# Optimization experiments

Hardware: AMD Instinct MI355X
Metric: run time of the kernel (lower is better)

The kernel has to match this reference:

```python
import jax, jax.numpy as jnp
import numpy as np

N = 131072      # H*W*batch = 128*128*8 features
D = 256         # feature_dim
P = 64          # proj_dim
E = 260096      # (2*H*W - H - W)*batch edges of the grid graph
G = 8192        # number of groups
SIM_THRESHOLD = 0.5


def setup_inputs() -> dict:
    key = jax.random.key(0)
    k0, k1, k2, k3 = jax.random.split(key, 4)
    features = jax.random.normal(k0, (N, D), dtype=jnp.float32)
    proj_W = jax.random.normal(k1, (D, P), dtype=jnp.float32) / np.sqrt(D)
    edge_index = jax.random.randint(k2, (2, E), 0, N, dtype=jnp.int64)
    group_ids = jax.random.randint(k3, (N,), 0, G, dtype=jnp.int64)
    return {
        "features": features,
        "proj_W": proj_W,
        "edge_index": edge_index,
        "group_ids": group_ids,
        "num_groups": G,
    }


def reference(features, proj_W, edge_index, group_ids, num_groups):
    # Projection: [N, D] @ [D, P] -> [N, P]
    proj = features @ proj_W
    # Pair comparison: gather both endpoints per edge, dot product per edge
    src, dst = edge_index[0], edge_index[1]
    sims = jnp.sum(proj[src] * proj[dst], axis=-1)            # [E]
    edge_logits = jax.nn.sigmoid(sims - SIM_THRESHOLD)        # [E]
    # Group mean pooling: scatter-add features per group, divide by size
    ones = jnp.ones((features.shape[0],), dtype=features.dtype)
    group_sums = jax.ops.segment_sum(features, group_ids, num_segments=num_groups)  # [G, D]
    group_sizes = jax.ops.segment_sum(ones, group_ids, num_segments=num_groups)     # [G]
    group_sizes = jnp.maximum(group_sizes, 1.0)
    group_means = group_sums / group_sizes[:, None]           # [G, D]
    return group_means, edge_logits
```

## Files before the change

kernel.cpp:

```cpp
#include <hip/hip_runtime.h>
#include <math.h>

constexpr int Nn = 131072;
constexpr int Dd = 256;
constexpr int Pp = 64;
constexpr int Gg = 8192;
constexpr int Ee = 260096;
constexpr float SIM_TH = 0.5f;

typedef _Float16 half8 __attribute__((ext_vector_type(8)));
typedef float floatx4 __attribute__((ext_vector_type(4)));

__global__ __launch_bounds__(256) void k_count_wfrag(
    const int* __restrict__ gid, int* __restrict__ cnt,
    const float* __restrict__ W, _Float16* __restrict__ Wf)
{
    const int i = blockIdx.x * 256 + threadIdx.x;
    atomicAdd(&cnt[gid[i]], 1);
    if (i < 16384) {
        const int j = i & 7;
        const int l = (i >> 3) & 63;
        const int t = (i >> 9) & 3;
        const int c = i >> 11;
        const int k = c * 32 + (l >> 4) * 8 + j;
        const int n = t * 16 + (l & 15);
        Wf[i] = (_Float16)W[k * Pp + n];
    }
}

__global__ __launch_bounds__(256) void k_proj(
    const float* __restrict__ A,
    const _Float16* __restrict__ Wf,
    _Float16* __restrict__ C)
{
    const int l = threadIdx.x & 63;
    const int w = threadIdx.x >> 6;
    const int rowbase = blockIdx.x * 64 + w * 16;
    const int am = l & 15;
    const int q  = l >> 4;

    const float* __restrict__ arow = A + (size_t)(rowbase + am) * Dd + q * 8;
    const half8* __restrict__ bfrag = reinterpret_cast<const half8*>(Wf) + l;

    floatx4 acc[4];
#pragma unroll
    for (int t = 0; t < 4; ++t) acc[t] = (floatx4){0.f, 0.f, 0.f, 0.f};

#pragma unroll
    for (int c = 0; c < 8; ++c) {
        const float4 fa = *reinterpret_cast<const float4*>(arow + c * 32);
        const float4 fb = *reinterpret_cast<const float4*>(arow + c * 32 + 4);
        half8 a;
        a[0] = (_Float16)fa.x; a[1] = (_Float16)fa.y;
        a[2] = (_Float16)fa.z; a[3] = (_Float16)fa.w;
        a[4] = (_Float16)fb.x; a[5] = (_Float16)fb.y;
        a[6] = (_Float16)fb.z; a[7] = (_Float16)fb.w;
        const half8 b0 = bfrag[(c * 4 + 0) * 64];
        const half8 b1 = bfrag[(c * 4 + 1) * 64];
        const half8 b2 = bfrag[(c * 4 + 2) * 64];
        const half8 b3 = bfrag[(c * 4 + 3) * 64];
        acc[0] = __builtin_amdgcn_mfma_f32_16x16x32_f16(a, b0, acc[0], 0, 0, 0);
        acc[1] = __builtin_amdgcn_mfma_f32_16x16x32_f16(a, b1, acc[1], 0, 0, 0);
        acc[2] = __builtin_amdgcn_mfma_f32_16x16x32_f16(a, b2, acc[2], 0, 0, 0);
        acc[3] = __builtin_amdgcn_mfma_f32_16x16x32_f16(a, b3, acc[3], 0, 0, 0);
    }

#pragma unroll
    for (int t = 0; t < 4; ++t) {
#pragma unroll
        for (int r = 0; r < 4; ++r) {
            C[(size_t)(rowbase + q * 4 + r) * Pp + t * 16 + (l & 15)] =
                (_Float16)acc[t][r];
        }
    }
}

__global__ __launch_bounds__(256) void k_scan(
    const int* __restrict__ cnt,
    int* __restrict__ offsets,
    int* __restrict__ cursor)
{
    __shared__ int lds[256];
    const int t = threadIdx.x;
    const int base = t * 32;

    int s = 0;
#pragma unroll
    for (int j = 0; j < 32; ++j) s += cnt[base + j];
    lds[t] = s;
    __syncthreads();

    int v = s;
    for (int off = 1; off < 256; off <<= 1) {
        int add = (t >= off) ? lds[t - off] : 0;
        __syncthreads();
        v += add;
        lds[t] = v;
        __syncthreads();
    }

    int run = v - s;
    for (int j = 0; j < 32; ++j) {
        offsets[base + j] = run;
        cursor[base + j]  = run;
        run += cnt[base + j];
    }
}

__global__ __launch_bounds__(256) void k_scatter_idx(
    const int* __restrict__ gid,
    int* __restrict__ cursor,
    int* __restrict__ bucket)
{
    const int i = blockIdx.x * 256 + threadIdx.x;
    const int p = atomicAdd(&cursor[gid[i]], 1);
    bucket[p] = i;
}

__global__ __launch_bounds__(256) void k_group_mean(
    const float* __restrict__ features,
    const int* __restrict__ bucket,
    const int* __restrict__ offsets,
    const int* __restrict__ cnt,
    float* __restrict__ out_means)
{
    const int lane = threadIdx.x & 63;
    const int g = blockIdx.x * 4 + (threadIdx.x >> 6);
    const int n = cnt[g];
    const int start = offsets[g];
    const int col = lane * 4;

    float4 s = make_float4(0.f, 0.f, 0.f, 0.f);
    int k = 0;
    for (; k + 8 <= n; k += 8) {
        int r[8];
#pragma unroll
        for (int u = 0; u < 8; ++u) r[u] = bucket[start + k + u];
        float4 f[8];
#pragma unroll
        for (int u = 0; u < 8; ++u)
            f[u] = *reinterpret_cast<const float4*>(features + (size_t)r[u] * Dd + col);
#pragma unroll
        for (int u = 0; u < 8; ++u) {
            s.x += f[u].x; s.y += f[u].y; s.z += f[u].z; s.w += f[u].w;
        }
    }
    for (; k < n; ++k) {
        const int r = bucket[start + k];
        const float4 f = *reinterpret_cast<const float4*>(features + (size_t)r * Dd + col);
        s.x += f.x; s.y += f.y; s.z += f.z; s.w += f.w;
    }
    const float inv = 1.0f / (float)max(n, 1);
    s.x *= inv; s.y *= inv; s.z *= inv; s.w *= inv;
    *reinterpret_cast<float4*>(out_means + (size_t)g * Dd + col) = s;
}

__global__ __launch_bounds__(256) void k_edges(
    const _Float16* __restrict__ proj,
    const int*      __restrict__ ei,
    float* __restrict__ out_logits)
{
    const int sub = threadIdx.x & 7;
    const int sg  = blockIdx.x * 32 + (threadIdx.x >> 3);
    const int e0  = sg * 4;

    int s[4], t[4];
#pragma unroll
    for (int u = 0; u < 4; ++u) { s[u] = ei[e0 + u]; t[u] = ei[Ee + e0 + u]; }

    half8 a[4], b[4];
#pragma unroll
    for (int u = 0; u < 4; ++u) {
        a[u] = *reinterpret_cast<const half8*>(proj + (size_t)s[u] * Pp + sub * 8);
        b[u] = *reinterpret_cast<const half8*>(proj + (size_t)t[u] * Pp + sub * 8);
    }

    float v[4];
#pragma unroll
    for (int u = 0; u < 4; ++u) {
        float acc = 0.f;
#pragma unroll
        for (int j = 0; j < 8; ++j)
            acc = fmaf((float)a[u][j], (float)b[u][j], acc);
        v[u] = acc;
    }

#pragma unroll
    for (int off = 4; off >= 1; off >>= 1) {
#pragma unroll
        for (int u = 0; u < 4; ++u) v[u] += __shfl_xor(v[u], off, 64);
    }

    if (sub < 4) {
        const float x = v[sub];
        out_logits[e0 + sub] = 1.0f / (1.0f + __expf(-(x - SIM_TH)));
    }
}

extern "C" void kernel_launch(void* const* d_in, const int* in_sizes, int n_in,
                              void* d_out, int out_size, void* d_ws, size_t ws_size,
                              hipStream_t stream)
{
    const float* features = (const float*)d_in[0];
    const float* W        = (const float*)d_in[1];
    const int*   ei       = (const int*)d_in[2];
    const int*   gid      = (const int*)d_in[3];

    float* out_means  = (float*)d_out;
    float* out_logits = out_means + (size_t)Gg * Dd;

    _Float16*  proj    = (_Float16*)d_ws;
    int*       bucket  = (int*)(proj + (size_t)Nn * Pp);
    int*       cnt     = bucket + Nn;
    int*       offsets = cnt + Gg;
    int*       cursor  = offsets + Gg;
    _Float16*  Wf      = (_Float16*)(cursor + Gg);

    hipMemsetAsync(cnt, 0, (size_t)Gg * sizeof(int), stream);

    hipLaunchKernelGGL(k_count_wfrag, dim3(Nn / 256), dim3(256), 0, stream,
                       gid, cnt, W, Wf);
    hipLaunchKernelGGL(k_proj, dim3(Nn / 64), dim3(256), 0, stream,
                       features, Wf, proj);
    hipLaunchKernelGGL(k_scan, dim3(1), dim3(256), 0, stream,
                       cnt, offsets, cursor);
    hipLaunchKernelGGL(k_scatter_idx, dim3(Nn / 256), dim3(256), 0, stream,
                       gid, cursor, bucket);
    hipLaunchKernelGGL(k_group_mean, dim3(Gg / 4), dim3(256), 0, stream,
                       features, bucket, offsets, cnt, out_means);
    hipLaunchKernelGGL(k_edges, dim3(Ee / 128), dim3(256), 0, stream,
                       proj, ei, out_logits);
}
```

Before: 256.8 us.

## Fuse projection GEMM into group-mean gather to read features once

Removes the separate projection kernel and computes the projection inside the group-mean kernel: each wave gathers its group's feature rows, accumulates the mean, stages fp16 copies in LDS in 16-row tiles, and runs MFMA to produce projected rows that are scattered back by original row index. This eliminates one full pass over the 128 MB feature matrix. In exchange, groups average 16 rows, so many tiles are partially padded and waste MFMA work. Proj writes become scattered 2-byte stores, and the LDS staging is done without an explicit barrier, which relies on wave-local ordering.

```diff
diff --git a/kernel.cpp b/kernel.cpp
--- a/kernel.cpp
+++ b/kernel.cpp
@@ -9,6 +9,7 @@
 constexpr float SIM_TH = 0.5f;
 
 typedef _Float16 half8 __attribute__((ext_vector_type(8)));
+typedef _Float16 half4 __attribute__((ext_vector_type(4)));
 typedef float floatx4 __attribute__((ext_vector_type(4)));
 
 __global__ __launch_bounds__(256) void k_count_wfrag(
@@ -28,53 +29,6 @@
     }
 }
 
-__global__ __launch_bounds__(256) void k_proj(
-    const float* __restrict__ A,
-    const _Float16* __restrict__ Wf,
-    _Float16* __restrict__ C)
-{
-    const int l = threadIdx.x & 63;
-    const int w = threadIdx.x >> 6;
-    const int rowbase = blockIdx.x * 64 + w * 16;
-    const int am = l & 15;
-    const int q  = l >> 4;
-
-    const float* __restrict__ arow = A + (size_t)(rowbase + am) * Dd + q * 8;
-    const half8* __restrict__ bfrag = reinterpret_cast<const half8*>(Wf) + l;
-
-    floatx4 acc[4];
-#pragma unroll
-    for (int t = 0; t < 4; ++t) acc[t] = (floatx4){0.f, 0.f, 0.f, 0.f};
-
-#pragma unroll
-    for (int c = 0; c < 8; ++c) {
-        const float4 fa = *reinterpret_cast<const float4*>(arow + c * 32);
-        const float4 fb = *reinterpret_cast<const float4*>(arow + c * 32 + 4);
-        half8 a;
-        a[0] = (_Float16)fa.x; a[1] = (_Float16)fa.y;
-        a[2] = (_Float16)fa.z; a[3] = (_Float16)fa.w;
-        a[4] = (_Float16)fb.x; a[5] = (_Float16)fb.y;
-        a[6] = (_Float16)fb.z; a[7] = (_Float16)fb.w;
-        const half8 b0 = bfrag[(c * 4 + 0) * 64];
-        const half8 b1 = bfrag[(c * 4 + 1) * 64];
-        const half8 b2 = bfrag[(c * 4 + 2) * 64];
-        const half8 b3 = bfrag[(c * 4 + 3) * 64];
-        acc[0] = __builtin_amdgcn_mfma_f32_16x16x32_f16(a, b0, acc[0], 0, 0, 0);
-        acc[1] = __builtin_amdgcn_mfma_f32_16x16x32_f16(a, b1, acc[1], 0, 0, 0);
-        acc[2] = __builtin_amdgcn_mfma_f32_16x16x32_f16(a, b2, acc[2], 0, 0, 0);
-        acc[3] = __builtin_amdgcn_mfma_f32_16x16x32_f16(a, b3, acc[3], 0, 0, 0);
-    }
-
-#pragma unroll
-    for (int t = 0; t < 4; ++t) {
-#pragma unroll
-        for (int r = 0; r < 4; ++r) {
-            C[(size_t)(rowbase + q * 4 + r) * Pp + t * 16 + (l & 15)] =
-                (_Float16)acc[t][r];
-        }
-    }
-}
-
 __global__ __launch_bounds__(256) void k_scan(
     const int* __restrict__ cnt,
     int* __restrict__ offsets,
@@ -117,42 +71,78 @@
     bucket[p] = i;
 }
 
-__global__ __launch_bounds__(256) void k_group_mean(
-    const float* __restrict__ features,
+__global__ __launch_bounds__(256) void k_fused(
+    const float* __restrict__ A,
+    const _Float16* __restrict__ Wf,
     const int* __restrict__ bucket,
     const int* __restrict__ offsets,
     const int* __restrict__ cnt,
+    _Float16* __restrict__ proj,
     float* __restrict__ out_means)
 {
-    const int lane = threadIdx.x & 63;
-    const int g = blockIdx.x * 4 + (threadIdx.x >> 6);
-    const int n = cnt[g];
+    __shared__ _Float16 lds[4][16][264];
+
+    const int l  = threadIdx.x & 63;
+    const int w  = threadIdx.x >> 6;
+    const int am = l & 15;
+    const int q  = l >> 4;
+    const int g  = blockIdx.x * 4 + w;
+
+    const int n     = cnt[g];
     const int start = offsets[g];
-    const int col = lane * 4;
-
-    float4 s = make_float4(0.f, 0.f, 0.f, 0.f);
-    int k = 0;
-    for (; k + 8 <= n; k += 8) {
-        int r[8];
-#pragma unroll
-        for (int u = 0; u < 8; ++u) r[u] = bucket[start + k + u];
-        float4 f[8];
-#pragma unroll
-        for (int u = 0; u < 8; ++u)
-            f[u] = *reinterpret_cast<const float4*>(features + (size_t)r[u] * Dd + col);
-#pragma unroll
-        for (int u = 0; u < 8; ++u) {
-            s.x += f[u].x; s.y += f[u].y; s.z += f[u].z; s.w += f[u].w;
+    const half8* __restrict__ bfrag = reinterpret_cast<const half8*>(Wf) + l;
+
+    float4 msum = make_float4(0.f, 0.f, 0.f, 0.f);
+
+    const int T = (n + 15) >> 4;
+    for (int t = 0; t < T; ++t) {
+#pragma unroll 4
+        for (int j = 0; j < 16; ++j) {
+            const int rj = t * 16 + j;
+            const bool v = rj < n;
+            const int row = bucket[start + (v ? rj : 0)];
+            float4 f = make_float4(0.f, 0.f, 0.f, 0.f);
+            if (v) f = *reinterpret_cast<const float4*>(A + (size_t)row * Dd + l * 4);
+            msum.x += f.x; msum.y += f.y; msum.z += f.z; msum.w += f.w;
+            half4 h;
+            h[0] = (_Float16)f.x; h[1] = (_Float16)f.y;
+            h[2] = (_Float16)f.z; h[3] = (_Float16)f.w;
+            *reinterpret_cast<half4*>(&lds[w][j][l * 4]) = h;
         }
-    }
-    for (; k < n; ++k) {
-        const int r = bucket[start + k];
-        const float4 f = *reinterpret_cast<const float4*>(features + (size_t)r * Dd + col);
-        s.x += f.x; s.y += f.y; s.z += f.z; s.w += f.w;
-    }
+
+        floatx4 acc[4];
+#pragma unroll
+        for (int tt = 0; tt < 4; ++tt) acc[tt] = (floatx4){0.f, 0.f, 0.f, 0.f};
+
+#pragma unroll
+        for (int c = 0; c < 8; ++c) {
+            const half8 a = *reinterpret_cast<const half8*>(&lds[w][am][c * 32 + q * 8]);
+            const half8 b0 = bfrag[(c * 4 + 0) * 64];
+            const half8 b1 = bfrag[(c * 4 + 1) * 64];
+            const half8 b2 = bfrag[(c * 4 + 2) * 64];
+            const half8 b3 = bfrag[(c * 4 + 3) * 64];
+            acc[0] = __builtin_amdgcn_mfma_f32_16x16x32_f16(a, b0, acc[0], 0, 0, 0);
+            acc[1] = __builtin_amdgcn_mfma_f32_16x16x32_f16(a, b1, acc[1], 0, 0, 0);
+            acc[2] = __builtin_amdgcn_mfma_f32_16x16x32_f16(a, b2, acc[2], 0, 0, 0);
+            acc[3] = __builtin_amdgcn_mfma_f32_16x16x32_f16(a, b3, acc[3], 0, 0, 0);
+        }
+
+#pragma unroll
+        for (int r = 0; r < 4; ++r) {
+            const int rr = t * 16 + q * 4 + r;
+            if (rr < n) {
+                const int prow = bucket[start + rr];
+                _Float16* pp = proj + (size_t)prow * Pp + (l & 15);
+#pragma unroll
+                for (int tt = 0; tt < 4; ++tt)
+                    pp[tt * 16] = (_Float16)acc[tt][r];
+            }
+        }
+    }
+
     const float inv = 1.0f / (float)max(n, 1);
-    s.x *= inv; s.y *= inv; s.z *= inv; s.w *= inv;
-    *reinterpret_cast<float4*>(out_means + (size_t)g * Dd + col) = s;
+    msum.x *= inv; msum.y *= inv; msum.z *= inv; msum.w *= inv;
+    *reinterpret_cast<float4*>(out_means + (size_t)g * Dd + l * 4) = msum;
 }
 
 __global__ __launch_bounds__(256) void k_edges(
@@ -220,14 +210,12 @@
 
     hipLaunchKernelGGL(k_count_wfrag, dim3(Nn / 256), dim3(256), 0, stream,
                        gid, cnt, W, Wf);
-    hipLaunchKernelGGL(k_proj, dim3(Nn / 64), dim3(256), 0, stream,
-                       features, Wf, proj);
     hipLaunchKernelGGL(k_scan, dim3(1), dim3(256), 0, stream,
                        cnt, offsets, cursor);
     hipLaunchKernelGGL(k_scatter_idx, dim3(Nn / 256), dim3(256), 0, stream,
                        gid, cursor, bucket);
-    hipLaunchKernelGGL(k_group_mean, dim3(Gg / 4), dim3(256), 0, stream,
-                       features, bucket, offsets, cnt, out_means);
+    hipLaunchKernelGGL(k_fused, dim3(Gg / 4), dim3(256), 0, stream,
+                       features, Wf, bucket, offsets, cnt, proj, out_means);
     hipLaunchKernelGGL(k_edges, dim3(Ee / 128), dim3(256), 0, stream,
                        proj, ei, out_logits);
 }
```

Result: slower. 313.3 us (+22.0%).

## Merge independent stages into two block-partitioned kernels to cut launch count

Applied to the files above, without the earlier changes.

The index scatter is folded into the projection kernel, and the group-mean and edge-logit kernels are combined into one. Each combined kernel picks its role by block index. Together with the scan reordering this goes from six launches to four, removing launch gaps and letting independent work run concurrently on the GPU. The cost is more register pressure in the combined kernels and possible imbalance between the two kinds of blocks.

```diff
diff --git a/kernel.cpp b/kernel.cpp
--- a/kernel.cpp
+++ b/kernel.cpp
@@ -28,14 +28,57 @@
     }
 }
 
-__global__ __launch_bounds__(256) void k_proj(
+__global__ __launch_bounds__(256) void k_scan(
+    const int* __restrict__ cnt,
+    int* __restrict__ offsets,
+    int* __restrict__ cursor)
+{
+    __shared__ int lds[256];
+    const int t = threadIdx.x;
+    const int base = t * 32;
+
+    int s = 0;
+#pragma unroll
+    for (int j = 0; j < 32; ++j) s += cnt[base + j];
+    lds[t] = s;
+    __syncthreads();
+
+    int v = s;
+    for (int off = 1; off < 256; off <<= 1) {
+        int add = (t >= off) ? lds[t - off] : 0;
+        __syncthreads();
+        v += add;
+        lds[t] = v;
+        __syncthreads();
+    }
+
+    int run = v - s;
+    for (int j = 0; j < 32; ++j) {
+        offsets[base + j] = run;
+        cursor[base + j]  = run;
+        run += cnt[base + j];
+    }
+}
+
+__global__ __launch_bounds__(256) void k_mid(
     const float* __restrict__ A,
     const _Float16* __restrict__ Wf,
-    _Float16* __restrict__ C)
-{
+    _Float16* __restrict__ proj,
+    const int* __restrict__ gid,
+    int* __restrict__ cursor,
+    int* __restrict__ bucket)
+{
+    if (blockIdx.x < 512) {
+        const int i = blockIdx.x * 256 + threadIdx.x;
+        const int p = atomicAdd(&cursor[gid[i]], 1);
+        bucket[p] = i;
+        return;
+    }
+    const int blk = blockIdx.x - 512;
+
     const int l = threadIdx.x & 63;
     const int w = threadIdx.x >> 6;
-    const int rowbase = blockIdx.x * 64 + w * 16;
+    const int rowbase = blk * 64 + w * 16;
     const int am = l & 15;
     const int q  = l >> 4;
 
@@ -69,99 +112,58 @@
     for (int t = 0; t < 4; ++t) {
 #pragma unroll
         for (int r = 0; r < 4; ++r) {
-            C[(size_t)(rowbase + q * 4 + r) * Pp + t * 16 + (l & 15)] =
+            proj[(size_t)(rowbase + q * 4 + r) * Pp + t * 16 + am] =
                 (_Float16)acc[t][r];
         }
     }
 }
 
-__global__ __launch_bounds__(256) void k_scan(
-    const int* __restrict__ cnt,
-    int* __restrict__ offsets,
-    int* __restrict__ cursor)
-{
-    __shared__ int lds[256];
-    const int t = threadIdx.x;
-    const int base = t * 32;
-
-    int s = 0;
-#pragma unroll
-    for (int j = 0; j < 32; ++j) s += cnt[base + j];
-    lds[t] = s;
-    __syncthreads();
-
-    int v = s;
-    for (int off = 1; off < 256; off <<= 1) {
-        int add = (t >= off) ? lds[t - off] : 0;
-        __syncthreads();
-        v += add;
-        lds[t] = v;
-        __syncthreads();
-    }
-
-    int run = v - s;
-    for (int j = 0; j < 32; ++j) {
-        offsets[base + j] = run;
-        cursor[base + j]  = run;
-        run += cnt[base + j];
-    }
-}
-
-__global__ __launch_bounds__(256) void k_scatter_idx(
-    const int* __restrict__ gid,
-    int* __restrict__ cursor,
-    int* __restrict__ bucket)
-{
-    const int i = blockIdx.x * 256 + threadIdx.x;
-    const int p = atomicAdd(&cursor[gid[i]], 1);
-    bucket[p] = i;
-}
-
-__global__ __launch_bounds__(256) void k_group_mean(
+__global__ __launch_bounds__(256) void k_tail(
     const float* __restrict__ features,
     const int* __restrict__ bucket,
     const int* __restrict__ offsets,
     const int* __restrict__ cnt,
-    float* __restrict__ out_means)
-{
-    const int lane = threadIdx.x & 63;
-    const int g = blockIdx.x * 4 + (threadIdx.x >> 6);
-    const int n = cnt[g];
-    const int start = offsets[g];
-    const int col = lane * 4;
-
-    float4 s = make_float4(0.f, 0.f, 0.f, 0.f);
-    int k = 0;
-    for (; k + 8 <= n; k += 8) {
-        int r[8];
-#pragma unroll
-        for (int u = 0; u < 8; ++u) r[u] = bucket[start + k + u];
-        float4 f[8];
-#pragma unroll
-        for (int u = 0; u < 8; ++u)
-            f[u] = *reinterpret_cast<const float4*>(features + (size_t)r[u] * Dd + col);
-#pragma unroll
-        for (int u = 0; u < 8; ++u) {
-            s.x += f[u].x; s.y += f[u].y; s.z += f[u].z; s.w += f[u].w;
+    float* __restrict__ out_means,
+    const _Float16* __restrict__ proj,
+    const int* __restrict__ ei,
+    float* __restrict__ out_logits)
+{
+    if (blockIdx.x < 2048) {
+        const int lane = threadIdx.x & 63;
+        const int g = blockIdx.x * 4 + (threadIdx.x >> 6);
+        const int n = cnt[g];
+        const int start = offsets[g];
+        const int col = lane * 4;
+
+        float4 s = make_float4(0.f, 0.f, 0.f, 0.f);
+        int k = 0;
+        for (; k + 8 <= n; k += 8) {
+            int r[8];
+#pragma unroll
+            for (int u = 0; u < 8; ++u) r[u] = bucket[start + k + u];
+            float4 f[8];
+#pragma unroll
+            for (int u = 0; u < 8; ++u)
+                f[u] = *reinterpret_cast<const float4*>(features + (size_t)r[u] * Dd + col);
+#pragma unroll
+            for (int u = 0; u < 8; ++u) {
+                s.x += f[u].x; s.y += f[u].y; s.z += f[u].z; s.w += f[u].w;
+            }
         }
-    }
-    for (; k < n; ++k) {
-        const int r = bucket[start + k];
-        const float4 f = *reinterpret_cast<const float4*>(features + (size_t)r * Dd + col);
-        s.x += f.x; s.y += f.y; s.z += f.z; s.w += f.w;
-    }
-    const float inv = 1.0f / (float)max(n, 1);
-    s.x *= inv; s.y *= inv; s.z *= inv; s.w *= inv;
-    *reinterpret_cast<float4*>(out_means + (size_t)g * Dd + col) = s;
-}
-
-__global__ __launch_bounds__(256) void k_edges(
-    const _Float16* __restrict__ proj,
-    const int*      __restrict__ ei,
-    float* __restrict__ out_logits)
-{
+        for (; k < n; ++k) {
+            const int r = bucket[start + k];
+            const float4 f = *reinterpret_cast<const float4*>(features + (size_t)r * Dd + col);
+            s.x += f.x; s.y += f.y; s.z += f.z; s.w += f.w;
+        }
+        const float inv = 1.0f / (float)max(n, 1);
+        s.x *= inv; s.y *= inv; s.z *= inv; s.w *= inv;
+        *reinterpret_cast<float4*>(out_means + (size_t)g * Dd + col) = s;
+        return;
+    }
+
+    const int bid = blockIdx.x - 2048;
     const int sub = threadIdx.x & 7;
-    const int sg  = blockIdx.x * 32 + (threadIdx.x >> 3);
+    const int sg  = bid * 32 + (threadIdx.x >> 3);
     const int e0  = sg * 4;
 
     int s[4], t[4];
@@ -220,14 +222,11 @@
 
     hipLaunchKernelGGL(k_count_wfrag, dim3(Nn / 256), dim3(256), 0, stream,
                        gid, cnt, W, Wf);
-    hipLaunchKernelGGL(k_proj, dim3(Nn / 64), dim3(256), 0, stream,
-                       features, Wf, proj);
     hipLaunchKernelGGL(k_scan, dim3(1), dim3(256), 0, stream,
                        cnt, offsets, cursor);
-    hipLaunchKernelGGL(k_scatter_idx, dim3(Nn / 256), dim3(256), 0, stream,
-                       gid, cursor, bucket);
-    hipLaunchKernelGGL(k_group_mean, dim3(Gg / 4), dim3(256), 0, stream,
-                       features, bucket, offsets, cnt, out_means);
-    hipLaunchKernelGGL(k_edges, dim3(Ee / 128), dim3(256), 0, stream,
+    hipLaunchKernelGGL(k_mid, dim3(512 + Nn / 64), dim3(256), 0, stream,
+                       features, Wf, proj, gid, cursor, bucket);
+    hipLaunchKernelGGL(k_tail, dim3(2048 + Ee / 128), dim3(256), 0, stream,
+                       features, bucket, offsets, cnt, out_means,
                        proj, ei, out_logits);
 }
```

Result: no change. 252.1 us (-1.8%).
